# Optimization experiments

Measured on AMD Instinct MI355X. Metric: run time of the kernel, lower is better.

Reference implementation:

```python
import jax, jax.numpy as jnp
import numpy as np


def setup_inputs() -> dict:
    key = jax.random.key(0)
    kq, kk, kv = jax.random.split(key, 3)
    B, H, S, D = 2, 16, 2048, 64
    q = jax.random.normal(kq, (B, H, S, D), dtype=jnp.float32)
    k = jax.random.normal(kk, (B, H, S, D), dtype=jnp.float32)
    v = jax.random.normal(kv, (B, H, S, D), dtype=jnp.float32)
    return {"q": q, "k": k, "v": v}


def reference(q, k, v):
    # Tiled attention without online softmax computes the same math as
    # standard scaled dot-product attention (non-causal).
    D = q.shape[-1]
    scale = 1.0 / jnp.sqrt(jnp.asarray(D, dtype=q.dtype))
    # scores: [B, H, Sq, Sk]
    scores = jnp.einsum("bhqd,bhkd->bhqk", q, k) * scale
    attn = jax.nn.softmax(scores, axis=-1)
    out = jnp.einsum("bhqk,bhkd->bhqd", attn, v)
    return out
```

## Files before the change

kernel.cpp:

```cpp
#include <hip/hip_runtime.h>
#include <hip/hip_bf16.h>
#include <stdint.h>


#define B_ 2
#define H_ 16
#define S_ 2048
#define D_ 64
#define BH_ (B_ * H_)
#define QBLK 128
#define KVBLK 64
#define NKV (S_ / KVBLK)
#define NPER (NKV / 2)

typedef __bf16 bf16_t;
typedef bf16_t bf16x8 __attribute__((ext_vector_type(8)));
typedef bf16_t bf16x4 __attribute__((ext_vector_type(4)));
typedef float f32x16 __attribute__((ext_vector_type(16)));
typedef uint32_t u32;

__device__ __forceinline__ f32x16 mfma32(bf16x8 a, bf16x8 b, f32x16 c) {
  return __builtin_amdgcn_mfma_f32_32x32x16_bf16(a, b, c, 0, 0, 0);
}

__device__ __forceinline__ u32 cvt_pk_bf16(float lo, float hi) {
  u32 r;
  asm("v_cvt_pk_bf16_f32 %0, %1, %2" : "=v"(r) : "v"(lo), "v"(hi));
  return r;
}

__device__ __forceinline__ void swap32(u32& x, u32& y) {
  asm("v_permlane32_swap_b32 %0, %1" : "+v"(x), "+v"(y));
}

__device__ __forceinline__ void gload_lds16(const bf16_t* g, bf16_t* l) {
  __builtin_amdgcn_global_load_lds(
      (const __attribute__((address_space(1))) unsigned int*)g,
      (__attribute__((address_space(3))) unsigned int*)l, 16, 0, 0);
}

__global__ void convert_k_kernel(const float* __restrict__ k, bf16_t* __restrict__ kb) {
  int i = blockIdx.x * blockDim.x + threadIdx.x;
  float4 x = ((const float4*)k)[i];
  bf16x4 o = { (bf16_t)x.x, (bf16_t)x.y, (bf16_t)x.z, (bf16_t)x.w };
  *(bf16x4*)(kb + (size_t)i * 4) = o;
}

__global__ void transpose_v_kernel(const float* __restrict__ v, bf16_t* __restrict__ vt) {
  __shared__ float tile[64][65];
  int bh = blockIdx.y, kt = blockIdx.x;
  const float* vp = v + ((size_t)bh * S_ + (size_t)kt * 64) * D_;
  int r0 = threadIdx.x >> 4;
  int c4 = (threadIdx.x & 15) * 4;
#pragma unroll
  for (int p = 0; p < 4; ++p) {
    int r = r0 + p * 16;
    float4 x = *(const float4*)(vp + (size_t)r * D_ + c4);
    tile[r][c4 + 0] = x.x; tile[r][c4 + 1] = x.y;
    tile[r][c4 + 2] = x.z; tile[r][c4 + 3] = x.w;
  }
  __syncthreads();
  bf16_t* op = vt + (size_t)bh * D_ * S_ + (size_t)kt * 64;
#pragma unroll
  for (int p = 0; p < 4; ++p) {
    int d = r0 + p * 16;
    bf16x4 o = { (bf16_t)tile[c4 + 0][d], (bf16_t)tile[c4 + 1][d],
                 (bf16_t)tile[c4 + 2][d], (bf16_t)tile[c4 + 3][d] };
    *(bf16x4*)(op + (size_t)d * S_ + c4) = o;
  }
}

__global__ __launch_bounds__(512, 4) void attn_kernel(
    const float* __restrict__ q, const bf16_t* __restrict__ kb,
    const bf16_t* __restrict__ vt, float* __restrict__ out) {
  const int bh = blockIdx.y;
  const int qt = blockIdx.x;
  const int tid = threadIdx.x;
  const int wid = tid >> 6;
  const int lane = tid & 63;
  const int wq = wid & 3;
  const int wkv = wid >> 2;
  const int l31 = lane & 31;
  const int hi = lane >> 5;

  __shared__ __align__(16) char smem[65536];
  bf16_t* kbuf = (bf16_t*)smem;
  bf16_t* vbuf = (bf16_t*)(smem + 32768);
  float* epi = (float*)smem;

  const bf16_t* kp = kb + (size_t)bh * S_ * D_;
  const bf16_t* vp = vt + (size_t)bh * D_ * S_;

  const int srow = tid >> 3;
  const int scol = (tid & 7) ^ (srow & 7);
  const int kofs = srow * D_ + scol * 8;
  const size_t vofs = (size_t)srow * S_ + scol * 8;
  const int ldst = wid * 512;

  const float qscale = 0.125f * 1.4426950408889634f;
  const int qrow = qt * QBLK + wq * 32 + l31;
  const float* qpr = q + ((size_t)bh * S_ + qrow) * D_;
  bf16x8 bq[4];
#pragma unroll
  for (int ks = 0; ks < 4; ++ks) {
    const float* p = qpr + ks * 16 + hi * 8;
    float4 x0 = *(const float4*)(p);
    float4 x1 = *(const float4*)(p + 4);
    bf16x8 a;
    a[0] = (bf16_t)(x0.x * qscale); a[1] = (bf16_t)(x0.y * qscale);
    a[2] = (bf16_t)(x0.z * qscale); a[3] = (bf16_t)(x0.w * qscale);
    a[4] = (bf16_t)(x1.x * qscale); a[5] = (bf16_t)(x1.y * qscale);
    a[6] = (bf16_t)(x1.z * qscale); a[7] = (bf16_t)(x1.w * qscale);
    bq[ks] = a;
  }

  float lsum = 0.f;
  f32x16 o0, o1;
#pragma unroll
  for (int r = 0; r < 16; ++r) { o0[r] = 0.f; o1[r] = 0.f; }

#pragma unroll
  for (int par = 0; par < 2; ++par) {
    gload_lds16(kp + (size_t)par * (KVBLK * D_) + kofs, kbuf + par * 4096 + ldst);
    gload_lds16(vp + (size_t)par * KVBLK + vofs, vbuf + par * 4096 + ldst);
  }
  __syncthreads();

  for (int p = 0; p < NPER; ++p) {
    if (p + 1 < NPER) {
      const int nb = ((p + 1) & 1) * 2;
#pragma unroll
      for (int par = 0; par < 2; ++par) {
        const int t = 2 * p + 2 + par;
        gload_lds16(kp + (size_t)t * (KVBLK * D_) + kofs,
                    kbuf + (nb + par) * 4096 + ldst);
        gload_lds16(vp + (size_t)t * KVBLK + vofs,
                    vbuf + (nb + par) * 4096 + ldst);
      }
    }

    const bf16_t* kt_ = kbuf + ((p & 1) * 2 + wkv) * 4096;
    const bf16_t* vt_ = vbuf + ((p & 1) * 2 + wkv) * 4096;

    u32 w[2][8];
#pragma unroll
    for (int sub = 0; sub < 2; ++sub) {
      f32x16 sv;
#pragma unroll
      for (int r = 0; r < 16; ++r) sv[r] = 0.f;
#pragma unroll
      for (int ks = 0; ks < 4; ++ks) {
        const int row = sub * 32 + l31;
        const int ch = (2 * ks + hi) ^ (row & 7);
        bf16x8 a = *(const bf16x8*)(kt_ + row * D_ + ch * 8);
        sv = mfma32(a, bq[ks], sv);
      }
#pragma unroll
      for (int b = 0; b < 4; ++b) {
        float e0 = __builtin_amdgcn_exp2f(sv[4 * b + 0]);
        float e1 = __builtin_amdgcn_exp2f(sv[4 * b + 1]);
        float e2 = __builtin_amdgcn_exp2f(sv[4 * b + 2]);
        float e3 = __builtin_amdgcn_exp2f(sv[4 * b + 3]);
        lsum += (e0 + e1) + (e2 + e3);
        w[sub][2 * b + 0] = cvt_pk_bf16(e0, e1);
        w[sub][2 * b + 1] = cvt_pk_bf16(e2, e3);
      }
#pragma unroll
      for (int kt2 = 0; kt2 < 2; ++kt2) {
        swap32(w[sub][4 * kt2 + 0], w[sub][4 * kt2 + 2]);
        swap32(w[sub][4 * kt2 + 1], w[sub][4 * kt2 + 3]);
      }
    }

#pragma unroll
    for (int sub = 0; sub < 2; ++sub)
#pragma unroll
      for (int kt2 = 0; kt2 < 2; ++kt2) {
        union { u32 u[4]; bf16x8 v; } pb;
        pb.u[0] = w[sub][4 * kt2 + 0]; pb.u[1] = w[sub][4 * kt2 + 1];
        pb.u[2] = w[sub][4 * kt2 + 2]; pb.u[3] = w[sub][4 * kt2 + 3];
        {
          const int row = l31;
          const int ch = (4 * sub + 2 * kt2 + hi) ^ (row & 7);
          bf16x8 a = *(const bf16x8*)(vt_ + row * KVBLK + ch * 8);
          o0 = mfma32(a, pb.v, o0);
        }
        {
          const int row = 32 + l31;
          const int ch = (4 * sub + 2 * kt2 + hi) ^ (row & 7);
          bf16x8 a = *(const bf16x8*)(vt_ + row * KVBLK + ch * 8);
          o1 = mfma32(a, pb.v, o1);
        }
      }

    __syncthreads();
  }

  if (wkv == 1) {
    float* e = epi + ((size_t)wq * 64 + lane) * 33;
#pragma unroll
    for (int r = 0; r < 16; ++r) { e[r] = o0[r]; e[16 + r] = o1[r]; }
    e[32] = lsum;
  }
  __syncthreads();
  if (wkv == 0) {
    const float* e = epi + ((size_t)wq * 64 + lane) * 33;
#pragma unroll
    for (int r = 0; r < 16; ++r) { o0[r] += e[r]; o1[r] += e[16 + r]; }
    lsum += e[32];
    float ltot = lsum + __shfl_xor(lsum, 32, 64);
    float inv = 1.f / ltot;
    float* op = out + ((size_t)bh * S_ + qrow) * D_;
#pragma unroll
    for (int b = 0; b < 4; ++b) {
      float4 w0 = { o0[4 * b + 0] * inv, o0[4 * b + 1] * inv,
                    o0[4 * b + 2] * inv, o0[4 * b + 3] * inv };
      *(float4*)(op + 8 * b + 4 * hi) = w0;
      float4 w1 = { o1[4 * b + 0] * inv, o1[4 * b + 1] * inv,
                    o1[4 * b + 2] * inv, o1[4 * b + 3] * inv };
      *(float4*)(op + 32 + 8 * b + 4 * hi) = w1;
    }
  }
}

extern "C" void kernel_launch(void* const* d_in, const int* in_sizes, int n_in,
                              void* d_out, int out_size, void* d_ws, size_t ws_size,
                              hipStream_t stream) {
  const float* q = (const float*)d_in[0];
  const float* k = (const float*)d_in[1];
  const float* v = (const float*)d_in[2];
  float* out = (float*)d_out;

  bf16_t* kb = (bf16_t*)d_ws;
  bf16_t* vt = kb + (size_t)BH_ * S_ * D_;

  int n4 = (BH_ * S_ * D_) / 4;
  convert_k_kernel<<<n4 / 256, 256, 0, stream>>>(k, kb);
  transpose_v_kernel<<<dim3(S_ / 64, BH_), 256, 0, stream>>>(v, vt);
  attn_kernel<<<dim3(S_ / QBLK, BH_), 512, 0, stream>>>(q, kb, vt, out);
}
```

Before: 58.87 us.

## Merge K/V prepass kernels, remap attention blocks for cache locality, add MFMA priority

The separate K-convert and V-transpose launches become one prepass kernel that picks its job from blockIdx.z, removing one launch and its gap. The attention grid is flattened and remapped so that consecutive block ids go to different (b,h) pairs spread across the XCDs, with each head's q-tiles grouped so its K/V is reused in the shared cache. s_setprio is raised around the MFMA sections so those waves get issue priority over the exp/convert work of other waves. These are three unrelated tweaks, and the remap mainly helps if it matches how the hardware actually distributes blocks to XCDs.

```diff
diff --git a/kernel.cpp b/kernel.cpp
--- a/kernel.cpp
+++ b/kernel.cpp
@@ -39,42 +39,52 @@
       (__attribute__((address_space(3))) unsigned int*)l, 16, 0, 0);
 }
 
-__global__ void convert_k_kernel(const float* __restrict__ k, bf16_t* __restrict__ kb) {
-  int i = blockIdx.x * blockDim.x + threadIdx.x;
-  float4 x = ((const float4*)k)[i];
-  bf16x4 o = { (bf16_t)x.x, (bf16_t)x.y, (bf16_t)x.z, (bf16_t)x.w };
-  *(bf16x4*)(kb + (size_t)i * 4) = o;
-}
-
-__global__ void transpose_v_kernel(const float* __restrict__ v, bf16_t* __restrict__ vt) {
+__global__ void prepass_kernel(const float* __restrict__ k,
+                               const float* __restrict__ v,
+                               bf16_t* __restrict__ kb,
+                               bf16_t* __restrict__ vt) {
   __shared__ float tile[64][65];
-  int bh = blockIdx.y, kt = blockIdx.x;
-  const float* vp = v + ((size_t)bh * S_ + (size_t)kt * 64) * D_;
-  int r0 = threadIdx.x >> 4;
-  int c4 = (threadIdx.x & 15) * 4;
-#pragma unroll
-  for (int p = 0; p < 4; ++p) {
-    int r = r0 + p * 16;
-    float4 x = *(const float4*)(vp + (size_t)r * D_ + c4);
-    tile[r][c4 + 0] = x.x; tile[r][c4 + 1] = x.y;
-    tile[r][c4 + 2] = x.z; tile[r][c4 + 3] = x.w;
-  }
-  __syncthreads();
-  bf16_t* op = vt + (size_t)bh * D_ * S_ + (size_t)kt * 64;
-#pragma unroll
-  for (int p = 0; p < 4; ++p) {
-    int d = r0 + p * 16;
-    bf16x4 o = { (bf16_t)tile[c4 + 0][d], (bf16_t)tile[c4 + 1][d],
-                 (bf16_t)tile[c4 + 2][d], (bf16_t)tile[c4 + 3][d] };
-    *(bf16x4*)(op + (size_t)d * S_ + c4) = o;
+  const int bh = blockIdx.y, kt = blockIdx.x;
+  if (blockIdx.z == 0) {
+    const float* src = k + ((size_t)bh * S_ + (size_t)kt * 64) * D_;
+    bf16_t* dst = kb + ((size_t)bh * S_ + (size_t)kt * 64) * D_;
+#pragma unroll
+    for (int i = 0; i < 4; ++i) {
+      int idx = i * 256 + threadIdx.x;
+      float4 x = ((const float4*)src)[idx];
+      bf16x4 o = { (bf16_t)x.x, (bf16_t)x.y, (bf16_t)x.z, (bf16_t)x.w };
+      *(bf16x4*)(dst + (size_t)idx * 4) = o;
+    }
+  } else {
+    const float* vp = v + ((size_t)bh * S_ + (size_t)kt * 64) * D_;
+    int r0 = threadIdx.x >> 4;
+    int c4 = (threadIdx.x & 15) * 4;
+#pragma unroll
+    for (int p = 0; p < 4; ++p) {
+      int r = r0 + p * 16;
+      float4 x = *(const float4*)(vp + (size_t)r * D_ + c4);
+      tile[r][c4 + 0] = x.x; tile[r][c4 + 1] = x.y;
+      tile[r][c4 + 2] = x.z; tile[r][c4 + 3] = x.w;
+    }
+    __syncthreads();
+    bf16_t* op = vt + (size_t)bh * D_ * S_ + (size_t)kt * 64;
+#pragma unroll
+    for (int p = 0; p < 4; ++p) {
+      int d = r0 + p * 16;
+      bf16x4 o = { (bf16_t)tile[c4 + 0][d], (bf16_t)tile[c4 + 1][d],
+                   (bf16_t)tile[c4 + 2][d], (bf16_t)tile[c4 + 3][d] };
+      *(bf16x4*)(op + (size_t)d * S_ + c4) = o;
+    }
   }
 }
 
 __global__ __launch_bounds__(512, 4) void attn_kernel(
     const float* __restrict__ q, const bf16_t* __restrict__ kb,
     const bf16_t* __restrict__ vt, float* __restrict__ out) {
-  const int bh = blockIdx.y;
-  const int qt = blockIdx.x;
+  const int bid = blockIdx.x;
+  const int g = bid >> 3;
+  const int bh = 4 * (bid & 7) + (g >> 4);
+  const int qt = g & 15;
   const int tid = threadIdx.x;
   const int wid = tid >> 6;
   const int lane = tid & 63;
@@ -148,6 +158,7 @@
       f32x16 sv;
 #pragma unroll
       for (int r = 0; r < 16; ++r) sv[r] = 0.f;
+      __builtin_amdgcn_s_setprio(1);
 #pragma unroll
       for (int ks = 0; ks < 4; ++ks) {
         const int row = sub * 32 + l31;
@@ -155,6 +166,7 @@
         bf16x8 a = *(const bf16x8*)(kt_ + row * D_ + ch * 8);
         sv = mfma32(a, bq[ks], sv);
       }
+      __builtin_amdgcn_s_setprio(0);
 #pragma unroll
       for (int b = 0; b < 4; ++b) {
         float e0 = __builtin_amdgcn_exp2f(sv[4 * b + 0]);
@@ -172,6 +184,7 @@
       }
     }
 
+    __builtin_amdgcn_s_setprio(1);
 #pragma unroll
     for (int sub = 0; sub < 2; ++sub)
 #pragma unroll
@@ -192,6 +205,7 @@
           o1 = mfma32(a, pb.v, o1);
         }
       }
+    __builtin_amdgcn_s_setprio(0);
 
     __syncthreads();
   }
@@ -234,8 +248,6 @@
   bf16_t* kb = (bf16_t*)d_ws;
   bf16_t* vt = kb + (size_t)BH_ * S_ * D_;
 
-  int n4 = (BH_ * S_ * D_) / 4;
-  convert_k_kernel<<<n4 / 256, 256, 0, stream>>>(k, kb);
-  transpose_v_kernel<<<dim3(S_ / 64, BH_), 256, 0, stream>>>(v, vt);
-  attn_kernel<<<dim3(S_ / QBLK, BH_), 512, 0, stream>>>(q, kb, vt, out);
-}
+  prepass_kernel<<<dim3(S_ / 64, BH_, 2), 256, 0, stream>>>(k, v, kb, vt);
+  attn_kernel<<<dim3(BH_ * (S_ / QBLK)), 512, 0, stream>>>(q, kb, vt, out);
+}
```

After: 57.21 us. 2.8% less time.
